# Kernel tuning notes

Hardware: AMD Instinct MI355X
Metric: run time of the kernel (lower is better)

Reference implementation:

```python
import jax, jax.numpy as jnp
import numpy as np

N = 100000          # nodes
F_IN = 500          # num_features
HID = 256           # hidden
C = 40              # out_classes
E = 2302585         # ~ N*ln(N)*ec, doubled (both directions) in spar_samp
ALPHA0 = 0.1        # att[0][0] = alpha*(1-alpha)**0


def setup_inputs() -> dict:
    key = jax.random.key(0)
    ks = jax.random.split(key, 8)
    x = jax.random.normal(ks[0], (N, F_IN), dtype=jnp.float32)
    W1 = jax.random.normal(ks[1], (F_IN, HID), dtype=jnp.float32) * (1.0 / np.sqrt(F_IN))
    b1 = jnp.zeros((HID,), dtype=jnp.float32)
    W2 = jax.random.normal(ks[2], (HID, C), dtype=jnp.float32) * (1.0 / np.sqrt(HID))
    b2 = jnp.zeros((C,), dtype=jnp.float32)
    edge_row = jax.random.randint(ks[3], (E,), 0, N, dtype=jnp.int64) if jax.config.jax_enable_x64 else jax.random.randint(ks[3], (E,), 0, N, dtype=jnp.int32)
    edge_col = jax.random.randint(ks[4], (E,), 0, N, dtype=edge_row.dtype)
    # sampled importance weights: deg^{-1/2}*deg^{-1/2}*(M/num_edgess) -> small positive floats
    edge_val = jax.random.uniform(ks[5], (E,), dtype=jnp.float32, minval=0.001, maxval=0.05)
    return {"x": x, "W1": W1, "b1": b1, "W2": W2, "b2": b2,
            "edge_row": edge_row, "edge_col": edge_col, "edge_val": edge_val}


def reference(x, W1, b1, W2, b2, edge_row, edge_col, edge_val):
    # eval mode: dropout is identity
    h = jax.nn.relu(x @ W1 + b1)          # [N, HID]
    h = h @ W2 + b2                       # [N, C]
    # sparse propagation: out[r] += val * h[c]  (scatter-add SpMM)
    msg = edge_val[:, None] * h[edge_col]            # [E, C] gather
    agg = jax.ops.segment_sum(msg, edge_row, num_segments=N)  # [N, C]
    out = h * ALPHA0 + agg
    return jax.nn.log_softmax(out, axis=1)
```

## Files before the change

kernel.cpp:

```cpp
#include <hip/hip_runtime.h>
#include <hip/hip_bf16.h>


#define N_NODES 100000
#define F_IN    500
#define HID     256
#define C_OUT   40
#define ALPHA0  0.1f
#define H2STRIDE 64

#define RPB     64
#define NBUCK   ((N_NODES + RPB - 1) / RPB)
#define NBUCKP  1568
#define NCH     256
#define BCAPL   1792

typedef short short8 __attribute__((ext_vector_type(8)));
typedef float f32x4  __attribute__((ext_vector_type(4)));

__device__ __forceinline__ short f2bf(float f) {
  union { float f; unsigned u; } x; x.f = f;
  unsigned r = x.u + 0x7fffu + ((x.u >> 16) & 1u);
  return (short)(r >> 16);
}
__device__ __forceinline__ float bf2f(short s) {
  union { unsigned u; float f; } x; x.u = ((unsigned)(unsigned short)s) << 16;
  return x.f;
}
__device__ __forceinline__ unsigned cvtpk(float lo, float hi) {
  unsigned r;
  asm("v_cvt_pk_bf16_f32 %0, %1, %2" : "=v"(r) : "v"(lo), "v"(hi));
  return r;
}
__device__ __forceinline__ void lbar() {
  asm volatile("s_waitcnt lgkmcnt(0)" ::: "memory");
  __builtin_amdgcn_s_barrier();
}
__device__ __forceinline__ void gll16(const float* g, const char* l) {
  __builtin_amdgcn_global_load_lds(
      (const __attribute__((address_space(1))) void*)g,
      (__attribute__((address_space(3))) void*)l, 16, 0, 0);
}

__global__ __launch_bounds__(256) void k_pack_weights(
    const float* __restrict__ W1, const float* __restrict__ W2,
    short* __restrict__ W1S, short* __restrict__ W2T)
{
  int i = blockIdx.x * 256 + threadIdx.x;
  if (i < 16*256*32) {
    int kc  = i >> 13;
    int idx = i & 8191;
    int n   = idx >> 5;
    int kk  = idx & 31;
    int k   = kc*32 + kk;
    float v = (k < F_IN) ? W1[k*HID + n] : 0.f;
    W1S[i] = f2bf(v);
  } else {
    int j = i - 16*256*32;
    if (j < 48*256) {
      int n = j >> 8;
      int k = j & 255;
      float v = (n < C_OUT) ? W2[k*C_OUT + n] : 0.f;
      W2T[j] = f2bf(v);
    }
  }
}

__global__ __launch_bounds__(256, 4) void k_fused_mlp(
    const float* __restrict__ x, const float* __restrict__ b1v,
    const float* __restrict__ b2v,
    const short* __restrict__ W1S, const short* __restrict__ W2T,
    short* __restrict__ h2b,
    const int* __restrict__ erow, const int* __restrict__ ecol,
    const float* __restrict__ eval, int* __restrict__ lofs,
    int2* __restrict__ sorted, int E, int CH)
{
  __shared__ __align__(16) char smem[32768];
  short (*Hl)[256] = (short(*)[256])smem;

  const int tid  = threadIdx.x;
  const int w    = tid >> 6;
  const int lane = tid & 63;
  const int lr   = lane & 15;
  const int quad = lane >> 4;
  const int row0 = blockIdx.x * 64;

  const int s_rl0 = (w*2)*8 + (lane>>3);
  const int s_rl1 = (w*2+1)*8 + (lane>>3);
  const int ksw   = ((lane&7) ^ ((lane>>3)&7)) * 4;
  const float* gp0 = x + (size_t)min(row0 + s_rl0, N_NODES-1) * F_IN;
  const float* gp1 = x + (size_t)min(row0 + s_rl1, N_NODES-1) * F_IN;
  const char* l0 = smem + (w*2)*1024;
  const char* l1 = smem + (w*2+1)*1024;

  f32x4 acc[4][4] = {};

  #pragma unroll
  for (int p = 0; p < 2; ++p) {
    int kb = p*32 + ksw;
    const float* a0 = (kb + 4 <= F_IN) ? gp0 + kb : x;
    const float* a1 = (kb + 4 <= F_IN) ? gp1 + kb : x;
    gll16(a0, l0 + p*8192);
    gll16(a1, l1 + p*8192);
  }

  const short* bbase = W1S + (w*64 + lr)*32 + quad*8;
  const int m2 = lr & 7;

  #pragma unroll
  for (int kc = 0; kc < 16; ++kc) {
    short8 bf4[4];
    #pragma unroll
    for (int t = 0; t < 4; ++t)
      bf4[t] = *(const short8*)(bbase + kc*8192 + t*16*32);
    __builtin_amdgcn_sched_barrier(0);

    if (kc < 14) {
      int kb = (kc+2)*32 + ksw;
      const float* a0 = (kb + 4 <= F_IN) ? gp0 + kb : x;
      const float* a1 = (kb + 4 <= F_IN) ? gp1 + kb : x;
      gll16(a0, l0 + ((kc+2)&3)*8192);
      gll16(a1, l1 + ((kc+2)&3)*8192);
      __builtin_amdgcn_sched_barrier(0);
      asm volatile("s_waitcnt vmcnt(8)" ::: "memory");
    } else if (kc == 14) {
      asm volatile("s_waitcnt vmcnt(6)" ::: "memory");
    } else {
      asm volatile("s_waitcnt vmcnt(4)" ::: "memory");
    }
    __builtin_amdgcn_s_barrier();

    const char* Abase = smem + (kc & 3)*8192;
    short8 af[4];
    #pragma unroll
    for (int t = 0; t < 4; ++t) {
      int rl = t*16 + lr;
      f32x4 u0 = *(const f32x4*)(Abase + rl*128 + (((quad*2  ) ^ m2) << 4));
      f32x4 u1 = *(const f32x4*)(Abase + rl*128 + (((quad*2+1) ^ m2) << 4));
      union { unsigned u[4]; short8 s; } pk;
      pk.u[0] = cvtpk(u0[0], u0[1]);
      pk.u[1] = cvtpk(u0[2], u0[3]);
      pk.u[2] = cvtpk(u1[0], u1[1]);
      pk.u[3] = cvtpk(u1[2], u1[3]);
      af[t] = pk.s;
    }

    #pragma unroll
    for (int rt = 0; rt < 4; ++rt)
      #pragma unroll
      for (int ct = 0; ct < 4; ++ct)
        acc[rt][ct] = __builtin_amdgcn_mfma_f32_16x16x32_bf16(af[rt], bf4[ct], acc[rt][ct], 0, 0, 0);
  }
  lbar();

  #pragma unroll
  for (int ct = 0; ct < 4; ++ct) {
    int col = w*64 + ct*16 + lr;
    int cg = col >> 3, ci = col & 7;
    float bias = b1v[col];
    #pragma unroll
    for (int rt = 0; rt < 4; ++rt) {
      #pragma unroll
      for (int r = 0; r < 4; ++r) {
        int row = rt*16 + quad*4 + r;
        float v = fmaxf(acc[rt][ct][r] + bias, 0.f);
        Hl[row][((cg ^ (row & 31)) << 3) | ci] = f2bf(v);
      }
    }
  }
  lbar();

  f32x4 acc2[3] = {};
  const int arow = w*16 + lr;
  #pragma unroll
  for (int kc2 = 0; kc2 < 8; ++kc2) {
    int gg = kc2*4 + quad;
    short8 a2 = *(const short8*)&Hl[arow][(gg ^ (arow & 31)) << 3];
    #pragma unroll
    for (int nt = 0; nt < 3; ++nt) {
      short8 b2 = *(const short8*)(W2T + (nt*16 + lr)*256 + kc2*32 + quad*8);
      acc2[nt] = __builtin_amdgcn_mfma_f32_16x16x32_bf16(a2, b2, acc2[nt], 0, 0, 0);
    }
  }

  #pragma unroll
  for (int nt = 0; nt < 3; ++nt) {
    int col = nt*16 + lr;
    float bias = (col < C_OUT) ? b2v[col] : 0.f;
    #pragma unroll
    for (int r = 0; r < 4; ++r) {
      int row = row0 + w*16 + quad*4 + r;
      if (row < N_NODES) {
        float v = (col < C_OUT) ? (acc2[nt][r] + bias) : 0.f;
        h2b[(long)row * H2STRIDE + col] = f2bf(v);
      }
    }
  }
  {
    int col = 48 + lr;
    #pragma unroll
    for (int r = 0; r < 4; ++r) {
      int row = row0 + w*16 + quad*4 + r;
      if (row < N_NODES) h2b[(long)row * H2STRIDE + col] = 0;
    }
  }

  if (blockIdx.x < NCH) {
    int cc = blockIdx.x;
    int* hcnt = (int*)smem;
    int* ssum = (int*)(smem + NBUCKP * 4);
    lbar();
    for (int b = tid; b < NBUCKP; b += 256) hcnt[b] = 0;
    __syncthreads();
    int e0 = cc * CH, e1 = min(E, e0 + CH);
    int g0 = e0 >> 2, g1 = e1 >> 2;
    const int4* rp = (const int4*)erow;
    if (e0 < e1) {
      for (int g = g0 + tid; g < g1; g += 256) {
        int4 r4 = rp[g];
        atomicAdd(&hcnt[r4.x >> 6], 1);
        atomicAdd(&hcnt[r4.y >> 6], 1);
        atomicAdd(&hcnt[r4.z >> 6], 1);
        atomicAdd(&hcnt[r4.w >> 6], 1);
      }
      for (int e = (g1 << 2) + tid; e < e1; e += 256)
        atomicAdd(&hcnt[erow[e] >> 6], 1);
    }
    __syncthreads();
    int base = tid * 8;
    int d[8];
    int s = 0;
    #pragma unroll
    for (int k = 0; k < 8; ++k) {
      d[k] = (base + k < NBUCKP) ? hcnt[base + k] : 0;
      s += d[k];
    }
    ssum[tid] = s;
    __syncthreads();
    for (int o = 1; o < 256; o <<= 1) {
      int u = (tid >= o) ? ssum[tid - o] : 0;
      __syncthreads();
      if (tid >= o) ssum[tid] += u;
      __syncthreads();
    }
    int run = ssum[tid] - s;
    int curv[8];
    #pragma unroll
    for (int k = 0; k < 8; ++k) {
      curv[k] = run;
      if (base + k < NBUCKP) lofs[(size_t)cc * NBUCKP + base + k] = run;
      run += d[k];
    }
    __syncthreads();
    #pragma unroll
    for (int k = 0; k < 8; ++k)
      if (base + k < NBUCKP) hcnt[base + k] = curv[k];
    __syncthreads();

    if (e0 < e1) {
      size_t obase = (size_t)cc * CH;
      const int4*   cp = (const int4*)ecol;
      const float4* vp = (const float4*)eval;
      for (int g = g0 + tid; g < g1; g += 256) {
        int4 r4 = rp[g];
        int4 c4 = cp[g];
        float4 v4 = vp[g];
        int p0 = atomicAdd(&hcnt[r4.x >> 6], 1);
        int p1 = atomicAdd(&hcnt[r4.y >> 6], 1);
        int p2 = atomicAdd(&hcnt[r4.z >> 6], 1);
        int p3 = atomicAdd(&hcnt[r4.w >> 6], 1);
        int2 cv;
        cv.x = c4.x | ((r4.x & 63) << 17); cv.y = __float_as_int(v4.x); sorted[obase + p0] = cv;
        cv.x = c4.y | ((r4.y & 63) << 17); cv.y = __float_as_int(v4.y); sorted[obase + p1] = cv;
        cv.x = c4.z | ((r4.z & 63) << 17); cv.y = __float_as_int(v4.z); sorted[obase + p2] = cv;
        cv.x = c4.w | ((r4.w & 63) << 17); cv.y = __float_as_int(v4.w); sorted[obase + p3] = cv;
      }
      for (int e = (g1 << 2) + tid; e < e1; e += 256) {
        int r = erow[e];
        int pos = atomicAdd(&hcnt[r >> 6], 1);
        int2 cv;
        cv.x = ecol[e] | ((r & 63) << 17);
        cv.y = __float_as_int(eval[e]);
        sorted[obase + pos] = cv;
      }
    }
  }
}

__global__ __launch_bounds__(256) void k_transpose(
    const int* __restrict__ lofs, int* __restrict__ lofsT)
{
  __shared__ int t[64][65];
  int cb = blockIdx.x & 3;
  int bb = blockIdx.x >> 2;
  int c0 = cb * 64, b0 = bb * 64;
  int j  = threadIdx.x & 63;
  int i0 = threadIdx.x >> 6;
  #pragma unroll
  for (int k = 0; k < 16; ++k) {
    int i = i0 + k * 4;
    int b = b0 + j;
    t[i][j] = (b <= NBUCK) ? lofs[(size_t)(c0 + i) * NBUCKP + b] : 0;
  }
  __syncthreads();
  #pragma unroll
  for (int k = 0; k < 16; ++k) {
    int i = i0 + k * 4;
    int b = b0 + i;
    if (b <= NBUCK) lofsT[(size_t)b * NCH + c0 + j] = t[j][i];
  }
}

__global__ __launch_bounds__(512) void k_csr_spmm(
    const int* __restrict__ lofsT, const int2* __restrict__ sorted,
    const short* __restrict__ h2b, float* __restrict__ out, int CH)
{
  __shared__ int2 eraw[BCAPL];
  __shared__ int2 eS[BCAPL];
  __shared__ int sA[NCH];
  __shared__ int cntc[NCH];
  __shared__ int cpos[NCH];
  __shared__ int h[RPB], roff[RPB], cur[RPB];
  int tid = threadIdx.x, b = blockIdx.x;
  int lane = tid & 63, w = tid >> 6;

  if (tid < NCH) {
    int a  = lofsT[(size_t)b * NCH + tid];
    int e2 = lofsT[(size_t)(b + 1) * NCH + tid];
    sA[tid]   = a;
    cntc[tid] = e2 - a;
    cpos[tid] = e2 - a;
  }
  if (tid < RPB) h[tid] = 0;
  __syncthreads();
  for (int o = 1; o < NCH; o <<= 1) {
    int u = (tid >= o && tid < NCH) ? cpos[tid - o] : 0;
    __syncthreads();
    if (tid >= o && tid < NCH) cpos[tid] += u;
    __syncthreads();
  }
  int cntT = min(cpos[NCH - 1], BCAPL);

  {
    int c    = tid & (NCH - 1);
    int half = tid >> 8;
    int srcb = c * CH + sA[c];
    int dstb = cpos[c] - cntc[c];
    int n    = cntc[c];
    for (int k = half; k < n; k += 2) {
      int p = dstb + k;
      if (p < BCAPL) {
        int2 cv = sorted[srcb + k];
        eraw[p] = cv;
        atomicAdd(&h[((unsigned)cv.x) >> 17], 1);
      }
    }
  }
  __syncthreads();
  if (w == 0) {
    int v = h[lane];
    int hv = v;
    #pragma unroll
    for (int o = 1; o < 64; o <<= 1) {
      int t = __shfl_up(v, o);
      if (lane >= o) v += t;
    }
    roff[lane] = v;
    cur[lane]  = v - hv;
  }
  __syncthreads();
  for (int i = tid; i < cntT; i += 512) {
    int2 cv = eraw[i];
    int p = atomicAdd(&cur[((unsigned)cv.x) >> 17], 1);
    if (p < BCAPL) eS[p] = cv;
  }
  __syncthreads();

  for (int rr = 0; rr < 8; ++rr) {
    int r = w * 8 + rr;
    int row = b * RPB + r;
    if (row >= N_NODES) continue;
    float acc = ALPHA0 * bf2f(h2b[(size_t)row * H2STRIDE + lane]);
    int e  = roff[r] - h[r];
    int ee = roff[r];
    for (; e + 7 < ee; e += 8) {
      int2 cc[8];
      float gg[8];
      #pragma unroll
      for (int j = 0; j < 8; ++j) cc[j] = eS[e + j];
      #pragma unroll
      for (int j = 0; j < 8; ++j)
        gg[j] = bf2f(h2b[(size_t)(cc[j].x & 0x1FFFF) * H2STRIDE + lane]);
      #pragma unroll
      for (int j = 0; j < 8; ++j) acc += __int_as_float(cc[j].y) * gg[j];
    }
    for (; e + 3 < ee; e += 4) {
      int2 c0 = eS[e], c1 = eS[e+1], c2 = eS[e+2], c3 = eS[e+3];
      float g0 = bf2f(h2b[(size_t)(c0.x & 0x1FFFF) * H2STRIDE + lane]);
      float g1 = bf2f(h2b[(size_t)(c1.x & 0x1FFFF) * H2STRIDE + lane]);
      float g2 = bf2f(h2b[(size_t)(c2.x & 0x1FFFF) * H2STRIDE + lane]);
      float g3 = bf2f(h2b[(size_t)(c3.x & 0x1FFFF) * H2STRIDE + lane]);
      acc += __int_as_float(c0.y) * g0;
      acc += __int_as_float(c1.y) * g1;
      acc += __int_as_float(c2.y) * g2;
      acc += __int_as_float(c3.y) * g3;
    }
    for (; e < ee; ++e) {
      int2 c0 = eS[e];
      acc += __int_as_float(c0.y) * bf2f(h2b[(size_t)(c0.x & 0x1FFFF) * H2STRIDE + lane]);
    }
    float m = (lane < C_OUT) ? acc : -INFINITY;
    #pragma unroll
    for (int o = 32; o > 0; o >>= 1) m = fmaxf(m, __shfl_xor(m, o));
    float ev = (lane < C_OUT) ? __expf(acc - m) : 0.f;
    float s = ev;
    #pragma unroll
    for (int o = 32; o > 0; o >>= 1) s += __shfl_xor(s, o);
    if (lane < C_OUT) out[(long)row * C_OUT + lane] = acc - m - __logf(s);
  }
}

extern "C" void kernel_launch(void* const* d_in, const int* in_sizes, int n_in,
                              void* d_out, int out_size, void* d_ws, size_t ws_size,
                              hipStream_t stream) {
  const float* x    = (const float*)d_in[0];
  const float* W1   = (const float*)d_in[1];
  const float* b1   = (const float*)d_in[2];
  const float* W2   = (const float*)d_in[3];
  const float* b2   = (const float*)d_in[4];
  const int*   erow = (const int*)d_in[5];
  const int*   ecol = (const int*)d_in[6];
  const float* eval = (const float*)d_in[7];
  const int E  = in_sizes[5];
  int CH = (E + NCH - 1) / NCH;
  CH = (CH + 3) & ~3;

  char* p = (char*)d_ws;
  short* h2b    = (short*)p;  p += (size_t)N_NODES * H2STRIDE * 2;
  short* W1S    = (short*)p;  p += (size_t)16*256*32 * 2;
  short* W2T    = (short*)p;  p += (size_t)48*256 * 2;
  int*   lofs   = (int*)p;    p += (size_t)NCH * NBUCKP * 4;
  int*   lofsT  = (int*)p;    p += (size_t)1600 * NCH * 4;
  int2*  sorted = (int2*)p;
  float* out = (float*)d_out;

  k_pack_weights<<<(16*256*32 + 48*256 + 255)/256, 256, 0, stream>>>(W1, W2, W1S, W2T);
  k_fused_mlp<<<(N_NODES + 63)/64, 256, 0, stream>>>(x, b1, b2, W1S, W2T, h2b,
                                                     erow, ecol, eval, lofs,
                                                     sorted, E, CH);
  k_transpose<<<4 * 25, 256, 0, stream>>>(lofs, lofsT);
  k_csr_spmm<<<NBUCK, 512, 0, stream>>>(lofsT, sorted, h2b, out, CH);
}
```

Baseline: 457.2 us.

## Split fused MLP work across 16 waves per block instead of 4

```diff
diff --git a/kernel.cpp b/kernel.cpp
--- a/kernel.cpp
+++ b/kernel.cpp
@@ -66,7 +66,7 @@
   }
 }
 
-__global__ __launch_bounds__(256, 4) void k_fused_mlp(
+__global__ __launch_bounds__(1024, 8) void k_fused_mlp(
     const float* __restrict__ x, const float* __restrict__ b1v,
     const float* __restrict__ b2v,
     const short* __restrict__ W1S, const short* __restrict__ W2T,
@@ -83,28 +83,24 @@
   const int lane = tid & 63;
   const int lr   = lane & 15;
   const int quad = lane >> 4;
+  const int rf   = w & 3;
+  const int cw   = w >> 2;
   const int row0 = blockIdx.x * 64;
 
-  const int s_rl0 = (w*2)*8 + (lane>>3);
-  const int s_rl1 = (w*2+1)*8 + (lane>>3);
-  const int ksw   = ((lane&7) ^ ((lane>>3)&7)) * 4;
-  const float* gp0 = x + (size_t)min(row0 + s_rl0, N_NODES-1) * F_IN;
-  const float* gp1 = x + (size_t)min(row0 + s_rl1, N_NODES-1) * F_IN;
-  const char* l0 = smem + (w*2)*1024;
-  const char* l1 = smem + (w*2+1)*1024;
-
-  f32x4 acc[4][4] = {};
-
-  #pragma unroll
-  for (int p = 0; p < 2; ++p) {
-    int kb = p*32 + ksw;
-    const float* a0 = (kb + 4 <= F_IN) ? gp0 + kb : x;
-    const float* a1 = (kb + 4 <= F_IN) ? gp1 + kb : x;
-    gll16(a0, l0 + p*8192);
-    gll16(a1, l1 + p*8192);
-  }
-
-  const short* bbase = W1S + (w*64 + lr)*32 + quad*8;
+  const bool stg  = (tid < 512);
+  const int  srow = tid >> 3;
+  const int  ksw  = ((tid & 7) ^ ((tid >> 3) & 7)) * 4;
+  const float* gp = x + (size_t)min(row0 + (stg ? srow : 0), N_NODES-1) * F_IN;
+  const char* lb  = smem + (w & 7) * 1024;
+
+  f32x4 acc[4] = {};
+
+  if (stg) {
+    gll16(gp + ksw,      lb);
+    gll16(gp + 32 + ksw, lb + 8192);
+  }
+
+  const short* bbase = W1S + (cw*64 + lr)*32 + quad*8;
   const int m2 = lr & 7;
 
   #pragma unroll
@@ -116,25 +112,24 @@
     __builtin_amdgcn_sched_barrier(0);
 
     if (kc < 14) {
-      int kb = (kc+2)*32 + ksw;
-      const float* a0 = (kb + 4 <= F_IN) ? gp0 + kb : x;
-      const float* a1 = (kb + 4 <= F_IN) ? gp1 + kb : x;
-      gll16(a0, l0 + ((kc+2)&3)*8192);
-      gll16(a1, l1 + ((kc+2)&3)*8192);
+      if (stg) {
+        int kb = (kc+2)*32 + ksw;
+        const float* a0 = (kb + 4 <= F_IN) ? gp + kb : x;
+        gll16(a0, lb + ((kc+2)&3)*8192);
+      }
       __builtin_amdgcn_sched_barrier(0);
-      asm volatile("s_waitcnt vmcnt(8)" ::: "memory");
+      asm volatile("s_waitcnt vmcnt(6)" ::: "memory");
     } else if (kc == 14) {
-      asm volatile("s_waitcnt vmcnt(6)" ::: "memory");
+      asm volatile("s_waitcnt vmcnt(5)" ::: "memory");
     } else {
       asm volatile("s_waitcnt vmcnt(4)" ::: "memory");
     }
     __builtin_amdgcn_s_barrier();
 
     const char* Abase = smem + (kc & 3)*8192;
-    short8 af[4];
-    #pragma unroll
-    for (int t = 0; t < 4; ++t) {
-      int rl = t*16 + lr;
+    short8 af;
+    {
+      int rl = rf*16 + lr;
       f32x4 u0 = *(const f32x4*)(Abase + rl*128 + (((quad*2  ) ^ m2) << 4));
       f32x4 u1 = *(const f32x4*)(Abase + rl*128 + (((quad*2+1) ^ m2) << 4));
       union { unsigned u[4]; short8 s; } pk;
@@ -142,65 +137,56 @@
       pk.u[1] = cvtpk(u0[2], u0[3]);
       pk.u[2] = cvtpk(u1[0], u1[1]);
       pk.u[3] = cvtpk(u1[2], u1[3]);
-      af[t] = pk.s;
-    }
-
-    #pragma unroll
-    for (int rt = 0; rt < 4; ++rt)
-      #pragma unroll
-      for (int ct = 0; ct < 4; ++ct)
-        acc[rt][ct] = __builtin_amdgcn_mfma_f32_16x16x32_bf16(af[rt], bf4[ct], acc[rt][ct], 0, 0, 0);
+      af = pk.s;
+    }
+
+    #pragma unroll
+    for (int ct = 0; ct < 4; ++ct)
+      acc[ct] = __builtin_amdgcn_mfma_f32_16x16x32_bf16(af, bf4[ct], acc[ct], 0, 0, 0);
   }
   lbar();
 
   #pragma unroll
   for (int ct = 0; ct < 4; ++ct) {
-    int col = w*64 + ct*16 + lr;
+    int col = cw*64 + ct*16 + lr;
     int cg = col >> 3, ci = col & 7;
     float bias = b1v[col];
     #pragma unroll
-    for (int rt = 0; rt < 4; ++rt) {
-      #pragma unroll
-      for (int r = 0; r < 4; ++r) {
-        int row = rt*16 + quad*4 + r;
-        float v = fmaxf(acc[rt][ct][r] + bias, 0.f);
-        Hl[row][((cg ^ (row & 31)) << 3) | ci] = f2bf(v);
-      }
+    for (int r = 0; r < 4; ++r) {
+      int row = rf*16 + quad*4 + r;
+      float v = fmaxf(acc[ct][r] + bias, 0.f);
+      Hl[row][((cg ^ (row & 31)) << 3) | ci] = f2bf(v);
     }
   }
   lbar();
 
-  f32x4 acc2[3] = {};
-  const int arow = w*16 + lr;
-  #pragma unroll
-  for (int kc2 = 0; kc2 < 8; ++kc2) {
-    int gg = kc2*4 + quad;
-    short8 a2 = *(const short8*)&Hl[arow][(gg ^ (arow & 31)) << 3];
-    #pragma unroll
-    for (int nt = 0; nt < 3; ++nt) {
+  if (w < 12) {
+    int rg = w & 3, nt = w >> 2;
+    f32x4 acc2 = {};
+    const int arow = rg*16 + lr;
+    #pragma unroll
+    for (int kc2 = 0; kc2 < 8; ++kc2) {
+      int gg = kc2*4 + quad;
+      short8 a2 = *(const short8*)&Hl[arow][(gg ^ (arow & 31)) << 3];
       short8 b2 = *(const short8*)(W2T + (nt*16 + lr)*256 + kc2*32 + quad*8);
-      acc2[nt] = __builtin_amdgcn_mfma_f32_16x16x32_bf16(a2, b2, acc2[nt], 0, 0, 0);
-    }
-  }
-
-  #pragma unroll
-  for (int nt = 0; nt < 3; ++nt) {
+      acc2 = __builtin_amdgcn_mfma_f32_16x16x32_bf16(a2, b2, acc2, 0, 0, 0);
+    }
     int col = nt*16 + lr;
     float bias = (col < C_OUT) ? b2v[col] : 0.f;
     #pragma unroll
     for (int r = 0; r < 4; ++r) {
-      int row = row0 + w*16 + quad*4 + r;
+      int row = row0 + rg*16 + quad*4 + r;
       if (row < N_NODES) {
-        float v = (col < C_OUT) ? (acc2[nt][r] + bias) : 0.f;
+        float v = (col < C_OUT) ? (acc2[r] + bias) : 0.f;
         h2b[(long)row * H2STRIDE + col] = f2bf(v);
       }
     }
-  }
-  {
+  } else {
+    int rg = w - 12;
     int col = 48 + lr;
     #pragma unroll
     for (int r = 0; r < 4; ++r) {
-      int row = row0 + w*16 + quad*4 + r;
+      int row = row0 + rg*16 + quad*4 + r;
       if (row < N_NODES) h2b[(long)row * H2STRIDE + col] = 0;
     }
   }
@@ -210,58 +196,48 @@
     int* hcnt = (int*)smem;
     int* ssum = (int*)(smem + NBUCKP * 4);
     lbar();
-    for (int b = tid; b < NBUCKP; b += 256) hcnt[b] = 0;
+    for (int b = tid; b < NBUCKP; b += 1024) hcnt[b] = 0;
     __syncthreads();
     int e0 = cc * CH, e1 = min(E, e0 + CH);
     int g0 = e0 >> 2, g1 = e1 >> 2;
     const int4* rp = (const int4*)erow;
     if (e0 < e1) {
-      for (int g = g0 + tid; g < g1; g += 256) {
+      for (int g = g0 + tid; g < g1; g += 1024) {
         int4 r4 = rp[g];
         atomicAdd(&hcnt[r4.x >> 6], 1);
         atomicAdd(&hcnt[r4.y >> 6], 1);
         atomicAdd(&hcnt[r4.z >> 6], 1);
         atomicAdd(&hcnt[r4.w >> 6], 1);
       }
-      for (int e = (g1 << 2) + tid; e < e1; e += 256)
+      for (int e = (g1 << 2) + tid; e < e1; e += 1024)
         atomicAdd(&hcnt[erow[e] >> 6], 1);
     }
     __syncthreads();
-    int base = tid * 8;
-    int d[8];
-    int s = 0;
-    #pragma unroll
-    for (int k = 0; k < 8; ++k) {
-      d[k] = (base + k < NBUCKP) ? hcnt[base + k] : 0;
-      s += d[k];
-    }
+    int base = tid * 2;
+    int d0 = (base     < NBUCKP) ? hcnt[base]     : 0;
+    int d1 = (base + 1 < NBUCKP) ? hcnt[base + 1] : 0;
+    int s = d0 + d1;
     ssum[tid] = s;
     __syncthreads();
-    for (int o = 1; o < 256; o <<= 1) {
+    for (int o = 1; o < 1024; o <<= 1) {
       int u = (tid >= o) ? ssum[tid - o] : 0;
       __syncthreads();
       if (tid >= o) ssum[tid] += u;
       __syncthreads();
     }
     int run = ssum[tid] - s;
-    int curv[8];
-    #pragma unroll
-    for (int k = 0; k < 8; ++k) {
-      curv[k] = run;
-      if (base + k < NBUCKP) lofs[(size_t)cc * NBUCKP + base + k] = run;
-      run += d[k];
-    }
-    __syncthreads();
-    #pragma unroll
-    for (int k = 0; k < 8; ++k)
-      if (base + k < NBUCKP) hcnt[base + k] = curv[k];
+    if (base < NBUCKP)     lofs[(size_t)cc * NBUCKP + base]     = run;
+    if (base + 1 < NBUCKP) lofs[(size_t)cc * NBUCKP + base + 1] = run + d0;
+    __syncthreads();
+    if (base < NBUCKP)     hcnt[base]     = run;
+    if (base + 1 < NBUCKP) hcnt[base + 1] = run + d0;
     __syncthreads();
 
     if (e0 < e1) {
       size_t obase = (size_t)cc * CH;
       const int4*   cp = (const int4*)ecol;
       const float4* vp = (const float4*)eval;
-      for (int g = g0 + tid; g < g1; g += 256) {
+      for (int g = g0 + tid; g < g1; g += 1024) {
         int4 r4 = rp[g];
         int4 c4 = cp[g];
         float4 v4 = vp[g];
@@ -275,7 +251,7 @@
         cv.x = c4.z | ((r4.z & 63) << 17); cv.y = __float_as_int(v4.z); sorted[obase + p2] = cv;
         cv.x = c4.w | ((r4.w & 63) << 17); cv.y = __float_as_int(v4.w); sorted[obase + p3] = cv;
       }
-      for (int e = (g1 << 2) + tid; e < e1; e += 256) {
+      for (int e = (g1 << 2) + tid; e < e1; e += 1024) {
         int r = erow[e];
         int pos = atomicAdd(&hcnt[r >> 6], 1);
         int2 cv;
@@ -445,9 +421,9 @@
   float* out = (float*)d_out;
 
   k_pack_weights<<<(16*256*32 + 48*256 + 255)/256, 256, 0, stream>>>(W1, W2, W1S, W2T);
-  k_fused_mlp<<<(N_NODES + 63)/64, 256, 0, stream>>>(x, b1, b2, W1S, W2T, h2b,
-                                                     erow, ecol, eval, lofs,
-                                                     sorted, E, CH);
+  k_fused_mlp<<<(N_NODES + 63)/64, 1024, 0, stream>>>(x, b1, b2, W1S, W2T, h2b,
+                                                      erow, ecol, eval, lofs,
+                                                      sorted, E, CH);
   k_transpose<<<4 * 25, 256, 0, stream>>>(lofs, lofsT);
   k_csr_spmm<<<NBUCK, 512, 0, stream>>>(lofsT, sorted, h2b, out, CH);
 }
```

Result: slower. 474.8 us (+3.8%).
